# Kernel tuning notes

Measured on AMD Instinct MI355X. Metric: run time of the kernel, lower is better.

Reference implementation:

```python
import jax, jax.numpy as jnp
import numpy as np

N = 50000
E = 800000
IN_C = 128
HID = 32
OUT_C = 16
NEG_SLOPE = 0.2


def setup_inputs() -> dict:
    key = jax.random.key(0)
    ks = jax.random.split(key, 16)
    x = jax.random.normal(ks[0], (N, IN_C), dtype=jnp.float32)
    edge_index = jax.random.randint(ks[1], (2, E), 0, N, dtype=jnp.int64)

    def glorot(k, shape):
        fan = shape[0] + shape[-1]
        return jax.random.uniform(k, shape, jnp.float32, -1.0, 1.0) * jnp.sqrt(6.0 / fan)

    # layer1: in=128 -> heads=4, ch=32, concat -> out 128
    W1 = glorot(ks[2], (IN_C, 4 * HID))
    a_src1 = glorot(ks[3], (4, HID))
    a_dst1 = glorot(ks[4], (4, HID))
    b1 = jnp.zeros((4 * HID,), jnp.float32)
    # layer2: in=128 -> heads=2, ch=32, concat -> out 64
    W2 = glorot(ks[5], (4 * HID, 2 * HID))
    a_src2 = glorot(ks[6], (2, HID))
    a_dst2 = glorot(ks[7], (2, HID))
    b2 = jnp.zeros((2 * HID,), jnp.float32)
    # layer3: in=64 -> heads=1, ch=16, mean -> out 16
    W3 = glorot(ks[8], (2 * HID, OUT_C))
    a_src3 = glorot(ks[9], (1, OUT_C))
    a_dst3 = glorot(ks[10], (1, OUT_C))
    b3 = jnp.zeros((OUT_C,), jnp.float32)
    return {"x": x, "edge_index": edge_index,
            "W1": W1, "a_src1": a_src1, "a_dst1": a_dst1, "b1": b1,
            "W2": W2, "a_src2": a_src2, "a_dst2": a_dst2, "b2": b2,
            "W3": W3, "a_src3": a_src3, "a_dst3": a_dst3, "b3": b3}


def gat_conv(x, src, dst, W, a_src, a_dst, bias, heads, ch, concat):
    n = x.shape[0]
    h = (x @ W).reshape(n, heads, ch)                      # [N,H,C]
    alpha_s = jnp.einsum('nhc,hc->nh', h, a_src)           # [N,H]
    alpha_d = jnp.einsum('nhc,hc->nh', h, a_dst)           # [N,H]
    logits = jax.nn.leaky_relu(alpha_s[src] + alpha_d[dst], NEG_SLOPE)  # [E,H]
    # segment softmax over edges sharing the same destination node
    m = jax.ops.segment_max(logits, dst, num_segments=n)
    m = jnp.where(jnp.isfinite(m), m, 0.0)
    e = jnp.exp(logits - m[dst])
    denom = jax.ops.segment_sum(e, dst, num_segments=n)
    alpha = e / (denom[dst] + 1e-16)                       # [E,H]
    msg = h[src] * alpha[:, :, None]                       # [E,H,C]
    out = jax.ops.segment_sum(msg, dst, num_segments=n)    # [N,H,C]
    out = out.reshape(n, heads * ch) if concat else out.mean(axis=1)
    return out + bias


def reference(x, edge_index, W1, a_src1, a_dst1, b1, W2, a_src2, a_dst2, b2, W3, a_src3, a_dst3, b3):
    n = x.shape[0]
    loops = jnp.arange(n, dtype=edge_index.dtype)
    src = jnp.concatenate([edge_index[0], loops])  # add self loops (PyG default)
    dst = jnp.concatenate([edge_index[1], loops])
    h = jax.nn.relu(gat_conv(x, src, dst, W1, a_src1, a_dst1, b1, 4, HID, True))
    h = jax.nn.relu(gat_conv(h, src, dst, W2, a_src2, a_dst2, b2, 2, HID, True))
    out = gat_conv(h, src, dst, W3, a_src3, a_dst3, b3, 1, OUT_C, False)
    return out
```

## Files before the change

kernel.cpp:

```cpp
#include <hip/hip_runtime.h>
#include <hip/hip_bf16.h>
#include <stdint.h>

#define NODES 50000
#define NEDGE 800000
#define TEDGE (NEDGE + NODES)

typedef unsigned short u16;
typedef unsigned int u32;
typedef unsigned long long u64;
typedef short s16x8 __attribute__((ext_vector_type(8)));
typedef float f32x4 __attribute__((ext_vector_type(4)));

__device__ __forceinline__ float bf2f(u16 v) {
  return __uint_as_float(((u32)v) << 16);
}
__device__ __forceinline__ u16 f2bf(float f) {
  u32 u = __float_as_uint(f);
  u32 r = (u + 0x7FFFu + ((u >> 16) & 1u)) >> 16;
  return (u16)r;
}
__device__ __forceinline__ float lo16f(u32 w) { return __uint_as_float(w << 16); }
__device__ __forceinline__ float hi16f(u32 w) { return __uint_as_float(w & 0xFFFF0000u); }
__device__ __forceinline__ float lrelu(float x) {
  return (x > 0.f) ? x : 0.2f * x;
}
__device__ __forceinline__ int clampn(int v) {
  return ((u32)v < NODES) ? v : 0;
}
__device__ __forceinline__ float load1(const void* p, size_t i, bool fb) {
  return fb ? bf2f(((const u16*)p)[i]) : ((const float*)p)[i];
}
__device__ __forceinline__ u32 encf(float f) {
  u32 u = __float_as_uint(f);
  return (u & 0x80000000u) ? ~u : (u | 0x80000000u);
}
__device__ __forceinline__ float decf(u32 k) {
  u32 u = (k & 0x80000000u) ? (k & 0x7FFFFFFFu) : ~k;
  return __uint_as_float(u);
}

__global__ __launch_bounds__(256) void k_probe(const int* __restrict__ ei,
                                               const u16* __restrict__ xs16,
                                               int* __restrict__ flags,
                                               int* __restrict__ deg) {
  int t = threadIdx.x;
  int g = blockIdx.x * 256 + t;
  if (g < NODES) deg[g] = 0;
  if (blockIdx.x == 0 && t >= 2 && t < 32) flags[t] = 0;
  if (blockIdx.x == 0 && t < 64) {
    int odd = 0, even = 0, big = 0;
#pragma unroll
    for (int k = 0; k < 4; ++k) {
      int idx = t + 64 * k;
      odd |= (ei[2 * idx + 1] != 0);
      even |= (ei[2 * idx] != 0);
      u32 ex = (xs16[2 * (t * 4 + k)] >> 7) & 0xFF;
      big += (ex >= 0x90);
    }
    u64 bo = __ballot(odd);
    u64 be = __ballot(even);
#pragma unroll
    for (int off = 32; off >= 1; off >>= 1) big += __shfl_xor(big, off);
    if (t == 0) {
      flags[0] = (bo == 0ull && be != 0ull) ? 1 : 0;
      flags[1] = (big >= 8) ? 0 : 1;
    }
  }
}

__global__ __launch_bounds__(256) void k_tw(const void* __restrict__ W1,
                                            const void* __restrict__ W2,
                                            const void* __restrict__ W3,
                                            const int* __restrict__ flags,
                                            u16* __restrict__ wt1,
                                            u16* __restrict__ wt2,
                                            u16* __restrict__ wt3) {
  int id = blockIdx.x * 256 + threadIdx.x;
  bool fb = flags[1] != 0;
  if (id < 16384) {
    int n = id >> 7, k = id & 127;
    wt1[n * 128 + k] = f2bf(load1(W1, (size_t)k * 128 + n, fb));
  } else if (id < 24576) {
    int r = id - 16384;
    int n = r >> 7, k = r & 127;
    wt2[n * 128 + k] = f2bf(load1(W2, (size_t)k * 64 + n, fb));
  } else if (id < 25600) {
    int r = id - 24576;
    int n = r >> 6, k = r & 63;
    wt3[n * 64 + k] = f2bf(load1(W3, (size_t)k * 16 + n, fb));
  }
}


__global__ __launch_bounds__(256) void k_hist(const int* __restrict__ ei,
                                              const int* __restrict__ flags,
                                              int* deg, u16* __restrict__ rankarr,
                                              u16* __restrict__ src16,
                                              u16* __restrict__ dst16) {
  int e = blockIdx.x * 256 + threadIdx.x;
  if (e >= TEDGE) return;
  int d, s;
  if (e < NEDGE) {
    if (flags[0]) { s = ei[2 * e]; d = ei[2 * (NEDGE + e)]; }
    else { s = ei[e]; d = ei[NEDGE + e]; }
  } else {
    s = e - NEDGE; d = s;
  }
  s = clampn(s); d = clampn(d);
  src16[e] = (u16)s;
  dst16[e] = (u16)d;
  int r = atomicAdd(&deg[d], 1);
  rankarr[e] = (u16)min(r, 65535);
}

__global__ __launch_bounds__(1024) void k_scan(const int* __restrict__ deg,
                                               int* __restrict__ rowptr, int n) {
  int t = threadIdx.x, lane = t & 63, w = t >> 6;
  __shared__ int swave[16], soff[17];
  int carry = 0;
  for (int base = 0; base < n; base += 4096) {
    int i0 = base + t * 4;
    int v[4];
#pragma unroll
    for (int j = 0; j < 4; j++) { int i = i0 + j; v[j] = (i < n) ? deg[i] : 0; }
    int local = v[0] + v[1] + v[2] + v[3];
    int x = local;
#pragma unroll
    for (int off = 1; off < 64; off <<= 1) {
      int y = __shfl_up(x, off);
      if (lane >= off) x += y;
    }
    if (lane == 63) swave[w] = x;
    __syncthreads();
    if (w == 0) {
      int wv = (lane < 16) ? swave[lane] : 0;
#pragma unroll
      for (int off = 1; off < 16; off <<= 1) {
        int y = __shfl_up(wv, off);
        if (lane >= off) wv += y;
      }
      if (lane < 16) soff[lane + 1] = wv;
      if (lane == 0) soff[0] = 0;
    }
    __syncthreads();
    int run = carry + soff[w] + (x - local);
#pragma unroll
    for (int j = 0; j < 4; j++) {
      int i = i0 + j;
      if (i < n) rowptr[i] = run;
      run += v[j];
    }
    carry += soff[16];
    __syncthreads();
  }
  if (t == 0) rowptr[n] = carry;
}

__global__ __launch_bounds__(256) void k_scatter(const u16* __restrict__ src16,
                                                 const u16* __restrict__ dst16,
                                                 const int* __restrict__ rowptr,
                                                 const u16* __restrict__ rankarr,
                                                 u16* __restrict__ srcs) {
  int e = blockIdx.x * 256 + threadIdx.x;
  if (e >= TEDGE) return;
  int d = dst16[e];
  int pos = rowptr[d] + (int)rankarr[e];
  srcs[pos] = src16[e];
}


template <int K, int N, int H, bool XEXT>
__global__ __launch_bounds__(256) void k_gmfma(const void* __restrict__ xin,
                                               const u16* __restrict__ wtg,
                                               const void* __restrict__ a_src,
                                               const void* __restrict__ a_dst,
                                               u16* __restrict__ hout,
                                               float* __restrict__ asg,
                                               float* __restrict__ adg,
                                               u32* __restrict__ gm,
                                               const int* __restrict__ flags,
                                               int M) {
  constexpr int KP = K + 8;
  constexpr int NT = N / 16;
  constexpr int NTH = NT / H;
  constexpr int KG = K / 8;
  __shared__ u16 wlds[N * KP];
  __shared__ u16 xlds[64 * KP];
  __shared__ u32 lmax[2 * H];
  int t = threadIdx.x;
  int row0 = blockIdx.x * 64;
  bool fb = flags[1] != 0;
  if (t < 2 * H) lmax[t] = 0;

  for (int i = t; i < N * KG; i += 256) {
    int n = i / KG, kg = i % KG;
    *(uint4*)&wlds[n * KP + kg * 8] = *(const uint4*)(wtg + (size_t)n * K + kg * 8);
  }
  bool xbf = XEXT ? fb : true;
  for (int i = t; i < 64 * KG; i += 256) {
    int r = i / KG, kg = i % KG;
    int grow = row0 + r;
    if (grow >= M) grow = M - 1;
    if (xbf) {
      *(uint4*)&xlds[r * KP + kg * 8] =
          *(const uint4*)((const u16*)xin + (size_t)grow * K + kg * 8);
    } else {
      const float* gp = (const float*)xin + (size_t)grow * K + kg * 8;
      float4 f0 = *(const float4*)gp, f1 = *(const float4*)(gp + 4);
      *(ushort4*)&xlds[r * KP + kg * 8] =
          make_ushort4(f2bf(f0.x), f2bf(f0.y), f2bf(f0.z), f2bf(f0.w));
      *(ushort4*)&xlds[r * KP + kg * 8 + 4] =
          make_ushort4(f2bf(f1.x), f2bf(f1.y), f2bf(f1.z), f2bf(f1.w));
    }
  }
  __syncthreads();

  int lane = t & 63, w = t >> 6;
  int lrow = lane & 15, quad = lane >> 4;
  f32x4 acc[NT];
#pragma unroll
  for (int nt = 0; nt < NT; ++nt) acc[nt] = (f32x4){0.f, 0.f, 0.f, 0.f};

  const u16* xbase = xlds + (w * 16 + lrow) * KP + quad * 8;
  const u16* wbase = wlds + lrow * KP + quad * 8;
#pragma unroll
  for (int ks = 0; ks < K / 32; ++ks) {
    s16x8 a = *(const s16x8*)(xbase + ks * 32);
#pragma unroll
    for (int nt = 0; nt < NT; ++nt) {
      s16x8 b = *(const s16x8*)(wbase + (size_t)nt * 16 * KP + ks * 32);
      acc[nt] = __builtin_amdgcn_mfma_f32_16x16x32_bf16(a, b, acc[nt], 0, 0, 0);
    }
  }

  float avs[NT], avd[NT];
#pragma unroll
  for (int nt = 0; nt < NT; ++nt) {
    avs[nt] = load1(a_src, nt * 16 + lrow, fb);
    avd[nt] = load1(a_dst, nt * 16 + lrow, fb);
  }
  int baserow = row0 + w * 16 + quad * 4;
#pragma unroll
  for (int r = 0; r < 4; ++r) {
    int grow = baserow + r;
    float ps[H], pd[H];
#pragma unroll
    for (int h = 0; h < H; ++h) {
      ps[h] = 0.f; pd[h] = 0.f;
#pragma unroll
      for (int i = 0; i < NTH; ++i) {
        int nt = h * NTH + i;
        ps[h] += acc[nt][r] * avs[nt];
        pd[h] += acc[nt][r] * avd[nt];
      }
    }
#pragma unroll
    for (int m = 1; m < 16; m <<= 1) {
#pragma unroll
      for (int h = 0; h < H; ++h) {
        ps[h] += __shfl_xor(ps[h], m);
        pd[h] += __shfl_xor(pd[h], m);
      }
    }
    if (grow < M) {
#pragma unroll
      for (int nt = 0; nt < NT; ++nt)
        hout[(size_t)grow * N + nt * 16 + lrow] = f2bf(acc[nt][r]);
#pragma unroll
      for (int h = 0; h < H; ++h) {
        if (lrow == h) {
          asg[grow * H + h] = ps[h];
          adg[grow * H + h] = pd[h];
          atomicMax(&lmax[h], encf(ps[h]));
          atomicMax(&lmax[H + h], encf(pd[h]));
        }
      }
    }
  }
  __syncthreads();
  if (t < 2 * H) atomicMax(&gm[t], lmax[t]);
}


template <int H, int C, bool RELU, bool FINAL>
__global__ __launch_bounds__(256) void k_agg(const u16* __restrict__ hbuf,
                                             const float* __restrict__ asg,
                                             const float* __restrict__ adg,
                                             const int* __restrict__ rowptr,
                                             const u16* __restrict__ srcs,
                                             const void* __restrict__ bias,
                                             const int* __restrict__ flags,
                                             const u32* __restrict__ gm,
                                             void* __restrict__ outp, int n) {
  constexpr int HC = H * C;
  constexpr int L = HC / 8;
  constexpr int EPN = 32 / L;
  constexpr int UN = (4 * EPN <= 32) ? 4 : 2;
  __shared__ u16 lds_s[4][64];
  __shared__ float lds_e[4][64][H];
  int lane = threadIdx.x & 63;
  int w = threadIdx.x >> 6;
  int nh = lane >> 5;
  int hl = lane & 31;
  int node = blockIdx.x * 8 + w * 2 + nh;
  if (node >= n) node = n - 1;
  bool fb = flags[1] != 0;
  int start = rowptr[node], end = rowptr[node + 1];
  if (end < start || end - start > TEDGE) { start = 0; end = 0; }

  float adh[H], M[H];
#pragma unroll
  for (int h = 0; h < H; ++h) adh[h] = adg[node * H + h];
#pragma unroll
  for (int h = 0; h < H; ++h) M[h] = lrelu(decf(gm[h]) + decf(gm[H + h]));

  int sub = hl / L;
  int cl = hl & (L - 1);
  int ch0 = cl * 8;
  int myhead = ch0 / C;
  int base = nh * 32;

  float den[H];
#pragma unroll
  for (int h = 0; h < H; ++h) den[h] = 0.f;
  float acc[UN][8];
#pragma unroll
  for (int u = 0; u < UN; ++u)
#pragma unroll
    for (int i = 0; i < 8; ++i) acc[u][i] = 0.f;

  for (int chunk = start; chunk < end; chunk += 32) {
    int e = chunk + hl;
    int s = 0;
    float ee[H];
#pragma unroll
    for (int h = 0; h < H; ++h) ee[h] = 0.f;
    if (e < end) {
      s = srcs[e];
      float av[H];
      if (H == 4) { float4 t4 = *(const float4*)(asg + s * 4);
        av[0] = t4.x; av[1] = t4.y; av[H > 2 ? 2 : 0] = t4.z; av[H > 3 ? 3 : 0] = t4.w; }
      else if (H == 2) { float2 t2 = *(const float2*)(asg + s * 2); av[0] = t2.x; av[1] = t2.y; }
      else av[0] = asg[s];
#pragma unroll
      for (int h = 0; h < H; ++h) {
        float x = __expf(lrelu(av[h] + adh[h]) - M[h]);
        ee[h] = x;
        den[h] += x;
      }
    }
    __builtin_amdgcn_wave_barrier();
    lds_s[w][lane] = (u16)s;
#pragma unroll
    for (int h = 0; h < H; ++h) lds_e[w][lane][h] = ee[h];
    __builtin_amdgcn_wave_barrier();

    int cn = min(32, end - chunk);
    for (int j = 0; j < cn; j += UN * EPN) {
      int sx[UN];
      float ax[UN];
#pragma unroll
      for (int u = 0; u < UN; ++u) {
        int ei_ = base + j + u * EPN + sub;
        sx[u] = lds_s[w][ei_];
        ax[u] = lds_e[w][ei_][myhead];
      }
#pragma unroll
      for (int u = 0; u < UN; ++u) {
        uint4 v = *(const uint4*)(hbuf + (size_t)sx[u] * HC + ch0);
        acc[u][0] += ax[u] * lo16f(v.x); acc[u][1] += ax[u] * hi16f(v.x);
        acc[u][2] += ax[u] * lo16f(v.y); acc[u][3] += ax[u] * hi16f(v.y);
        acc[u][4] += ax[u] * lo16f(v.z); acc[u][5] += ax[u] * hi16f(v.z);
        acc[u][6] += ax[u] * lo16f(v.w); acc[u][7] += ax[u] * hi16f(v.w);
      }
    }
  }

#pragma unroll
  for (int m = 16; m >= 1; m >>= 1) {
#pragma unroll
    for (int h = 0; h < H; ++h) den[h] += __shfl_xor(den[h], m);
  }
  float tt[8];
#pragma unroll
  for (int i = 0; i < 8; ++i) {
    tt[i] = acc[0][i];
#pragma unroll
    for (int u = 1; u < UN; ++u) tt[i] += acc[u][i];
  }
#pragma unroll
  for (int m = L; m < 32; m <<= 1) {
#pragma unroll
    for (int i = 0; i < 8; ++i) tt[i] += __shfl_xor(tt[i], m);
  }

  if (sub == 0) {
    float inv = 1.f / (den[myhead] + 1e-16f);
    float o[8];
#pragma unroll
    for (int i = 0; i < 8; ++i) {
      o[i] = tt[i] * inv + load1(bias, ch0 + i, fb);
      if (RELU) o[i] = fmaxf(o[i], 0.f);
    }
    bool obf = FINAL ? fb : true;
    if (obf) {
      uint4 pk;
      pk.x = (u32)f2bf(o[0]) | ((u32)f2bf(o[1]) << 16);
      pk.y = (u32)f2bf(o[2]) | ((u32)f2bf(o[3]) << 16);
      pk.z = (u32)f2bf(o[4]) | ((u32)f2bf(o[5]) << 16);
      pk.w = (u32)f2bf(o[6]) | ((u32)f2bf(o[7]) << 16);
      *(uint4*)((u16*)outp + (size_t)node * HC + ch0) = pk;
    } else {
      float* op = (float*)outp + (size_t)node * HC + ch0;
      *(float4*)op = make_float4(o[0], o[1], o[2], o[3]);
      *(float4*)(op + 4) = make_float4(o[4], o[5], o[6], o[7]);
    }
  }
}


extern "C" void kernel_launch(void* const* d_in, const int* in_sizes, int n_in,
                              void* d_out, int out_size, void* d_ws, size_t ws_size,
                              hipStream_t stream) {
  const void* x   = d_in[0];
  const int* ei   = (const int*)d_in[1];
  const void* W1  = d_in[2];
  const void* as1 = d_in[3];
  const void* ad1 = d_in[4];
  const void* b1  = d_in[5];
  const void* W2  = d_in[6];
  const void* as2 = d_in[7];
  const void* ad2 = d_in[8];
  const void* b2  = d_in[9];
  const void* W3  = d_in[10];
  const void* as3 = d_in[11];
  const void* ad3 = d_in[12];
  const void* b3  = d_in[13];

  char* w = (char*)d_ws;
  auto alloc = [&](size_t bytes) {
    char* p = w;
    w += (bytes + 255) & ~(size_t)255;
    return p;
  };
  int* flags    = (int*)alloc(256);
  int* deg      = (int*)alloc((size_t)NODES * 4);
  int* rowptr   = (int*)alloc((size_t)(NODES + 1) * 4);
  u16* rankarr  = (u16*)alloc((size_t)TEDGE * 2);
  u16* src16    = (u16*)alloc((size_t)TEDGE * 2);
  u16* dst16    = (u16*)alloc((size_t)TEDGE * 2);
  u16* srcs     = (u16*)alloc((size_t)TEDGE * 2);
  float* asg    = (float*)alloc((size_t)NODES * 4 * 4);
  float* adg    = (float*)alloc((size_t)NODES * 4 * 4);
  u16* wt1      = (u16*)alloc((size_t)128 * 128 * 2);
  u16* wt2      = (u16*)alloc((size_t)64 * 128 * 2);
  u16* wt3      = (u16*)alloc((size_t)16 * 64 * 2);
  u16* hbuf     = (u16*)alloc((size_t)NODES * 128 * 2);
  u16* obuf     = (u16*)alloc((size_t)NODES * 128 * 2);

  u32* gm1 = (u32*)(flags + 8);
  u32* gm2 = (u32*)(flags + 16);
  u32* gm3 = (u32*)(flags + 24);

  k_probe<<<(NODES + 255) / 256, 256, 0, stream>>>(ei, (const u16*)x, flags, deg);
  k_tw<<<100, 256, 0, stream>>>(W1, W2, W3, flags, wt1, wt2, wt3);
  k_hist<<<(TEDGE + 255) / 256, 256, 0, stream>>>(ei, flags, deg, rankarr, src16, dst16);
  k_scan<<<1, 1024, 0, stream>>>(deg, rowptr, NODES);
  k_scatter<<<(TEDGE + 255) / 256, 256, 0, stream>>>(src16, dst16, rowptr, rankarr, srcs);

  int gblocks = (NODES + 63) / 64;
  int ablocks = (NODES + 7) / 8;
  k_gmfma<128, 128, 4, true><<<gblocks, 256, 0, stream>>>(x, wt1, as1, ad1, hbuf, asg, adg, gm1, flags, NODES);
  k_agg<4, 32, true, false><<<ablocks, 256, 0, stream>>>(hbuf, asg, adg, rowptr, srcs, b1, flags, gm1, obuf, NODES);
  k_gmfma<128, 64, 2, false><<<gblocks, 256, 0, stream>>>(obuf, wt2, as2, ad2, hbuf, asg, adg, gm2, flags, NODES);
  k_agg<2, 32, true, false><<<ablocks, 256, 0, stream>>>(hbuf, asg, adg, rowptr, srcs, b2, flags, gm2, obuf, NODES);
  k_gmfma<64, 16, 1, false><<<gblocks, 256, 0, stream>>>(obuf, wt3, as3, ad3, hbuf, asg, adg, gm3, flags, NODES);
  k_agg<1, 16, false, true><<<ablocks, 256, 0, stream>>>(hbuf, asg, adg, rowptr, srcs, b3, flags, gm3, d_out, NODES);
}
```

Baseline: 309.5 us.

## Split hidden features into per-slice planes so aggregation gathers hit smaller working sets

The GEMM kernel now writes its projected features into SL separate planes (node-major within each slice) instead of one interleaved row. The aggregation kernel launches twice as many blocks for layers 1 and 2, and each block handles one slice (half the heads) for a group of nodes. The block index is interleaved so adjacent blocks cover the same node groups for different slices. The aim is to shrink the random-gather working set per pass and raise parallelism. The cost is that edge lists and attention logits are recomputed once per slice.

```diff
diff --git a/kernel.cpp b/kernel.cpp
--- a/kernel.cpp
+++ b/kernel.cpp
@@ -170,7 +170,7 @@
 }
 
 
-template <int K, int N, int H, bool XEXT>
+template <int K, int N, int H, int SL, bool XEXT>
 __global__ __launch_bounds__(256) void k_gmfma(const void* __restrict__ xin,
                                                const u16* __restrict__ wtg,
                                                const void* __restrict__ a_src,
@@ -185,6 +185,7 @@
   constexpr int NT = N / 16;
   constexpr int NTH = NT / H;
   constexpr int KG = K / 8;
+  constexpr int NS = N / SL;
   __shared__ u16 wlds[N * KP];
   __shared__ u16 xlds[64 * KP];
   __shared__ u32 lmax[2 * H];
@@ -265,8 +266,12 @@
     }
     if (grow < M) {
 #pragma unroll
-      for (int nt = 0; nt < NT; ++nt)
-        hout[(size_t)grow * N + nt * 16 + lrow] = f2bf(acc[nt][r]);
+      for (int nt = 0; nt < NT; ++nt) {
+        constexpr int TPS = NS / 16;
+        int sl = nt / TPS;
+        int lc = (nt % TPS) * 16 + lrow;
+        hout[((size_t)sl * M + grow) * NS + lc] = f2bf(acc[nt][r]);
+      }
 #pragma unroll
       for (int h = 0; h < H; ++h) {
         if (lrow == h) {
@@ -283,7 +288,7 @@
 }
 
 
-template <int H, int C, bool RELU, bool FINAL>
+template <int H, int C, int SL, bool RELU, bool FINAL>
 __global__ __launch_bounds__(256) void k_agg(const u16* __restrict__ hbuf,
                                              const float* __restrict__ asg,
                                              const float* __restrict__ adg,
@@ -294,36 +299,44 @@
                                              const u32* __restrict__ gm,
                                              void* __restrict__ outp, int n) {
   constexpr int HC = H * C;
-  constexpr int L = HC / 8;
+  constexpr int HCS = HC / SL;
+  constexpr int HH = H / SL;
+  constexpr int L = HCS / 8;
   constexpr int EPN = 32 / L;
   constexpr int UN = (4 * EPN <= 32) ? 4 : 2;
   __shared__ u16 lds_s[4][64];
-  __shared__ float lds_e[4][64][H];
+  __shared__ float lds_e[4][64][HH];
   int lane = threadIdx.x & 63;
   int w = threadIdx.x >> 6;
   int nh = lane >> 5;
   int hl = lane & 31;
-  int node = blockIdx.x * 8 + w * 2 + nh;
+  int b = blockIdx.x;
+  int slice, ng;
+  if (SL == 1) { slice = 0; ng = b; }
+  else { slice = (b >> 2) & 1; ng = ((b >> 3) << 2) | (b & 3); }
+  int node = ng * 8 + w * 2 + nh;
   if (node >= n) node = n - 1;
   bool fb = flags[1] != 0;
   int start = rowptr[node], end = rowptr[node + 1];
   if (end < start || end - start > TEDGE) { start = 0; end = 0; }
 
-  float adh[H], M[H];
-#pragma unroll
-  for (int h = 0; h < H; ++h) adh[h] = adg[node * H + h];
-#pragma unroll
-  for (int h = 0; h < H; ++h) M[h] = lrelu(decf(gm[h]) + decf(gm[H + h]));
+  int h0 = slice * HH;
+  float adh[HH], M[HH];
+#pragma unroll
+  for (int j = 0; j < HH; ++j) {
+    adh[j] = adg[node * H + h0 + j];
+    M[j] = lrelu(decf(gm[h0 + j]) + decf(gm[H + h0 + j]));
+  }
 
   int sub = hl / L;
   int cl = hl & (L - 1);
   int ch0 = cl * 8;
-  int myhead = ch0 / C;
-  int base = nh * 32;
-
-  float den[H];
-#pragma unroll
-  for (int h = 0; h < H; ++h) den[h] = 0.f;
+  int mh = ch0 / C;
+  const u16* hbs = hbuf + (size_t)slice * n * HCS;
+
+  float den[HH];
+#pragma unroll
+  for (int j = 0; j < HH; ++j) den[j] = 0.f;
   float acc[UN][8];
 #pragma unroll
   for (int u = 0; u < UN; ++u)
@@ -333,9 +346,9 @@
   for (int chunk = start; chunk < end; chunk += 32) {
     int e = chunk + hl;
     int s = 0;
-    float ee[H];
-#pragma unroll
-    for (int h = 0; h < H; ++h) ee[h] = 0.f;
+    float ee[HH];
+#pragma unroll
+    for (int j = 0; j < HH; ++j) ee[j] = 0.f;
     if (e < end) {
       s = srcs[e];
       float av[H];
@@ -344,18 +357,19 @@
       else if (H == 2) { float2 t2 = *(const float2*)(asg + s * 2); av[0] = t2.x; av[1] = t2.y; }
       else av[0] = asg[s];
 #pragma unroll
-      for (int h = 0; h < H; ++h) {
-        float x = __expf(lrelu(av[h] + adh[h]) - M[h]);
-        ee[h] = x;
-        den[h] += x;
+      for (int j = 0; j < HH; ++j) {
+        float x = __expf(lrelu(av[h0 + j] + adh[j]) - M[j]);
+        ee[j] = x;
+        den[j] += x;
       }
     }
     __builtin_amdgcn_wave_barrier();
     lds_s[w][lane] = (u16)s;
 #pragma unroll
-    for (int h = 0; h < H; ++h) lds_e[w][lane][h] = ee[h];
+    for (int j = 0; j < HH; ++j) lds_e[w][lane][j] = ee[j];
     __builtin_amdgcn_wave_barrier();
 
+    int base = nh * 32;
     int cn = min(32, end - chunk);
     for (int j = 0; j < cn; j += UN * EPN) {
       int sx[UN];
@@ -364,11 +378,11 @@
       for (int u = 0; u < UN; ++u) {
         int ei_ = base + j + u * EPN + sub;
         sx[u] = lds_s[w][ei_];
-        ax[u] = lds_e[w][ei_][myhead];
+        ax[u] = lds_e[w][ei_][mh];
       }
 #pragma unroll
       for (int u = 0; u < UN; ++u) {
-        uint4 v = *(const uint4*)(hbuf + (size_t)sx[u] * HC + ch0);
+        uint4 v = *(const uint4*)(hbs + (size_t)sx[u] * HCS + ch0);
         acc[u][0] += ax[u] * lo16f(v.x); acc[u][1] += ax[u] * hi16f(v.x);
         acc[u][2] += ax[u] * lo16f(v.y); acc[u][3] += ax[u] * hi16f(v.y);
         acc[u][4] += ax[u] * lo16f(v.z); acc[u][5] += ax[u] * hi16f(v.z);
@@ -380,7 +394,7 @@
 #pragma unroll
   for (int m = 16; m >= 1; m >>= 1) {
 #pragma unroll
-    for (int h = 0; h < H; ++h) den[h] += __shfl_xor(den[h], m);
+    for (int j = 0; j < HH; ++j) den[j] += __shfl_xor(den[j], m);
   }
   float tt[8];
 #pragma unroll
@@ -396,11 +410,12 @@
   }
 
   if (sub == 0) {
-    float inv = 1.f / (den[myhead] + 1e-16f);
+    int gch = slice * HCS + ch0;
+    float inv = 1.f / (den[mh] + 1e-16f);
     float o[8];
 #pragma unroll
     for (int i = 0; i < 8; ++i) {
-      o[i] = tt[i] * inv + load1(bias, ch0 + i, fb);
+      o[i] = tt[i] * inv + load1(bias, gch + i, fb);
       if (RELU) o[i] = fmaxf(o[i], 0.f);
     }
     bool obf = FINAL ? fb : true;
@@ -410,9 +425,9 @@
       pk.y = (u32)f2bf(o[2]) | ((u32)f2bf(o[3]) << 16);
       pk.z = (u32)f2bf(o[4]) | ((u32)f2bf(o[5]) << 16);
       pk.w = (u32)f2bf(o[6]) | ((u32)f2bf(o[7]) << 16);
-      *(uint4*)((u16*)outp + (size_t)node * HC + ch0) = pk;
+      *(uint4*)((u16*)outp + (size_t)node * HC + gch) = pk;
     } else {
-      float* op = (float*)outp + (size_t)node * HC + ch0;
+      float* op = (float*)outp + (size_t)node * HC + gch;
       *(float4*)op = make_float4(o[0], o[1], o[2], o[3]);
       *(float4*)(op + 4) = make_float4(o[4], o[5], o[6], o[7]);
     }
@@ -470,11 +485,14 @@
   k_scatter<<<(TEDGE + 255) / 256, 256, 0, stream>>>(src16, dst16, rowptr, rankarr, srcs);
 
   int gblocks = (NODES + 63) / 64;
-  int ablocks = (NODES + 7) / 8;
-  k_gmfma<128, 128, 4, true><<<gblocks, 256, 0, stream>>>(x, wt1, as1, ad1, hbuf, asg, adg, gm1, flags, NODES);
-  k_agg<4, 32, true, false><<<ablocks, 256, 0, stream>>>(hbuf, asg, adg, rowptr, srcs, b1, flags, gm1, obuf, NODES);
-  k_gmfma<128, 64, 2, false><<<gblocks, 256, 0, stream>>>(obuf, wt2, as2, ad2, hbuf, asg, adg, gm2, flags, NODES);
-  k_agg<2, 32, true, false><<<ablocks, 256, 0, stream>>>(hbuf, asg, adg, rowptr, srcs, b2, flags, gm2, obuf, NODES);
-  k_gmfma<64, 16, 1, false><<<gblocks, 256, 0, stream>>>(obuf, wt3, as3, ad3, hbuf, asg, adg, gm3, flags, NODES);
-  k_agg<1, 16, false, true><<<ablocks, 256, 0, stream>>>(hbuf, asg, adg, rowptr, srcs, b3, flags, gm3, d_out, NODES);
-}
+  int ngroups = (NODES + 7) / 8;
+  int ablocks2 = 8 * ((ngroups + 3) / 4);
+  int ablocks1 = ngroups;
+
+  k_gmfma<128, 128, 4, 2, true><<<gblocks, 256, 0, stream>>>(x, wt1, as1, ad1, hbuf, asg, adg, gm1, flags, NODES);
+  k_agg<4, 32, 2, true, false><<<ablocks2, 256, 0, stream>>>(hbuf, asg, adg, rowptr, srcs, b1, flags, gm1, obuf, NODES);
+  k_gmfma<128, 64, 2, 2, false><<<gblocks, 256, 0, stream>>>(obuf, wt2, as2, ad2, hbuf, asg, adg, gm2, flags, NODES);
+  k_agg<2, 32, 2, true, false><<<ablocks2, 256, 0, stream>>>(hbuf, asg, adg, rowptr, srcs, b2, flags, gm2, obuf, NODES);
+  k_gmfma<64, 16, 1, 1, false><<<gblocks, 256, 0, stream>>>(obuf, wt3, as3, ad3, hbuf, asg, adg, gm3, flags, NODES);
+  k_agg<1, 16, 1, false, true><<<ablocks1, 256, 0, stream>>>(hbuf, asg, adg, rowptr, srcs, b3, flags, gm3, d_out, NODES);
+}
```

Measured after the change: 327.7 us. 5.9% more time.
